# Performance work log

Hardware: AMD Instinct MI355X
Metric: run time of the kernel (lower is better)

The kernel has to match this reference:

```python
import jax, jax.numpy as jnp
import numpy as np

B, L, H, E, K = 64, 200, 256, 8, 2
LN_EPS = 1e-5

def setup_inputs() -> dict:
    key = jax.random.key(0)
    ks = jax.random.split(key, 24)
    r = lambda k, *s: jax.random.normal(k, s, dtype=jnp.float32)
    w = lambda k, *s: 0.02 * jax.random.normal(k, s, dtype=jnp.float32)
    return {
        'text_emb': r(ks[0], B, L, H),
        'img_emb': r(ks[1], B, L, H),
        'item_emb': r(ks[2], B, L, H),
        'noise_t': r(ks[3], B, L, H),
        'noise_i': r(ks[4], B, L, H),
        'W_mu_t': w(ks[5], H, H), 'b_mu_t': jnp.zeros((H,), jnp.float32),
        'W_sg_t': w(ks[6], H, H), 'b_sg_t': jnp.zeros((H,), jnp.float32),
        'W_mu_i': w(ks[7], H, H), 'b_mu_i': jnp.zeros((H,), jnp.float32),
        'W_sg_i': w(ks[8], H, H), 'b_sg_i': jnp.zeros((H,), jnp.float32),
        'W_gate': w(ks[9], H, E), 'b_gate': jnp.zeros((E,), jnp.float32),
        'W_texp': w(ks[10], E, H, H), 'b_texp': jnp.zeros((E, H), jnp.float32),
        'W_iexp': w(ks[11], E, H, H), 'b_iexp': jnp.zeros((E, H), jnp.float32),
        'W_fuse': w(ks[12], 2 * H, H), 'b_fuse': jnp.zeros((H,), jnp.float32),
        'ln_g': jnp.ones((H,), jnp.float32), 'ln_b': jnp.zeros((H,), jnp.float32),
    }

def _topk_routing(z, W_gate, b_gate):
    # softmax over experts, keep top-k, renormalize (matches torch scatter_ version)
    weights = jax.nn.softmax(z @ W_gate + b_gate, axis=-1)   # [B,L,E]
    top_w, idx = jax.lax.top_k(weights, K)                   # [B,L,K]
    sparse = jnp.sum(jax.nn.one_hot(idx, E, dtype=weights.dtype) * top_w[..., None], axis=-2)
    return sparse / (jnp.sum(sparse, axis=-1, keepdims=True) + 1e-8)

def _layernorm(x, g, b):
    mu = jnp.mean(x, axis=-1, keepdims=True)
    var = jnp.mean(jnp.square(x - mu), axis=-1, keepdims=True)
    return (x - mu) * jax.lax.rsqrt(var + LN_EPS) * g + b

def reference(text_emb, img_emb, item_emb, noise_t, noise_i,
              W_mu_t, b_mu_t, W_sg_t, b_sg_t, W_mu_i, b_mu_i, W_sg_i, b_sg_i,
              W_gate, b_gate, W_texp, b_texp, W_iexp, b_iexp,
              W_fuse, b_fuse, ln_g, ln_b):
    # VAE-style reparameterization per modality
    t_mu = text_emb @ W_mu_t + b_mu_t
    t_sigma = jnp.exp(text_emb @ W_sg_t + b_sg_t)
    i_mu = img_emb @ W_mu_i + b_mu_i
    i_sigma = jnp.exp(img_emb @ W_sg_i + b_sg_i)
    t_z = t_mu + t_sigma * noise_t
    i_z = i_mu + i_sigma * noise_i
    # top-k gating
    t_gate = _topk_routing(t_z, W_gate, b_gate)   # [B,L,E]
    i_gate = _topk_routing(i_z, W_gate, b_gate)
    # dense all-expert stack + gated combine
    t_experts = jnp.einsum('blh,ehd->bled', t_z, W_texp) + b_texp  # [B,L,E,H]
    t_out = jnp.einsum('bled,ble->bld', t_experts, t_gate)
    i_experts = jnp.einsum('blh,ehd->bled', i_z, W_iexp) + b_iexp
    i_out = jnp.einsum('bled,ble->bld', i_experts, i_gate)
    # fusion: Linear(2H->H) -> LayerNorm -> ReLU, residual with item_emb
    cat = jnp.concatenate([t_out, i_out], axis=-1)
    fused = jax.nn.relu(_layernorm(cat @ W_fuse + b_fuse, ln_g, ln_b))
    fusion = item_emb + fused
    return fusion, t_mu, t_sigma, i_mu, i_sigma
```

## Files before the change

kernel.cpp:

```cpp
#include <hip/hip_runtime.h>
#include <hip/hip_bf16.h>
#include <math.h>

#define NTOK 12800
#define HD 256
#define SOUT (NTOK * HD)

typedef __attribute__((ext_vector_type(8))) short short8_t;
typedef __attribute__((ext_vector_type(4))) float f32x4;

__device__ __forceinline__ unsigned short f2b(float f) {
    union { float f; unsigned u; } v; v.f = f;
    unsigned r = (v.u + 0x7FFFu + ((v.u >> 16) & 1u)) >> 16;
    return (unsigned short)r;
}
__device__ __forceinline__ float b2f(unsigned short s) {
    union { unsigned u; float f; } v; v.u = ((unsigned)s) << 16;
    return v.f;
}
__device__ __forceinline__ void glds16(const void* g, void* l) {
    __builtin_amdgcn_global_load_lds(
        (const __attribute__((address_space(1))) void*)g,
        (__attribute__((address_space(3))) void*)l, 16, 0, 0);
}
__device__ __forceinline__ short8_t add_bf16x8(short8_t a, short8_t b) {
    union { unsigned short u[8]; short8_t v; } ua, ub, r;
    ua.v = a; ub.v = b;
#pragma unroll
    for (int i = 0; i < 8; ++i) r.u[i] = f2b(b2f(ua.u[i]) + b2f(ub.u[i]));
    return r.v;
}
__device__ __forceinline__ void split8(const float* s, short8_t* hi, short8_t* lo) {
    const float4 v0 = *reinterpret_cast<const float4*>(s);
    const float4 v1 = *reinterpret_cast<const float4*>(s + 4);
    const float x[8] = { v0.x, v0.y, v0.z, v0.w, v1.x, v1.y, v1.z, v1.w };
    union { unsigned short u[8]; short8_t v; } qh, ql;
#pragma unroll
    for (int c = 0; c < 8; ++c) {
        qh.u[c] = f2b(x[c]);
        ql.u[c] = f2b(x[c] - b2f(qh.u[c]));
    }
    *hi = qh.v;
    *lo = ql.v;
}

__global__ __launch_bounds__(256) void prepW_kernel(
    const float* __restrict__ W_texp, const float* __restrict__ W_iexp,
    const float* __restrict__ W_mu_t, const float* __restrict__ W_sg_t,
    const float* __restrict__ W_mu_i, const float* __restrict__ W_sg_i,
    const float* __restrict__ W_fuse,
    unsigned short* __restrict__ wt_t, unsigned short* __restrict__ wt_i,
    unsigned short* __restrict__ wt_f,
    unsigned short* __restrict__ wpk_th, unsigned short* __restrict__ wpk_tl,
    unsigned short* __restrict__ wpk_ih, unsigned short* __restrict__ wpk_il)
{
    const int z = blockIdx.y;
    const float* src;
    unsigned short* dsth;
    unsigned short* dstl = nullptr;
    int dstride = 256, koff = 0, rowoff = 0;
    if (z < 8)       { src = W_texp + (size_t)z * 65536;       dsth = wt_t + (size_t)z * 65536; }
    else if (z < 16) { src = W_iexp + (size_t)(z - 8) * 65536; dsth = wt_i + (size_t)(z - 8) * 65536; }
    else if (z == 16){ src = W_mu_t; dsth = wpk_th; dstl = wpk_tl; }
    else if (z == 17){ src = W_sg_t; dsth = wpk_th; dstl = wpk_tl; rowoff = 256; }
    else if (z == 18){ src = W_mu_i; dsth = wpk_ih; dstl = wpk_il; }
    else if (z == 19){ src = W_sg_i; dsth = wpk_ih; dstl = wpk_il; rowoff = 256; }
    else if (z == 20){ src = W_fuse;         dsth = wt_f; dstride = 512; koff = 0;   }
    else             { src = W_fuse + 65536; dsth = wt_f; dstride = 512; koff = 256; }

    const int tk = (blockIdx.x >> 2) * 64;
    const int td = (blockIdx.x & 3) * 64;
    __shared__ float T[64][68];
    const int t = threadIdx.x;
    {
        const int r = t >> 2, c0 = (t & 3) * 16;
        const float* s = &src[(size_t)(tk + r) * 256 + td + c0];
#pragma unroll
        for (int j = 0; j < 4; ++j)
            *reinterpret_cast<float4*>(&T[r][c0 + j * 4]) =
                *reinterpret_cast<const float4*>(&s[j * 4]);
    }
    __syncthreads();
    {
        const int d = t & 63, kc = (t >> 6) * 16;
        union { unsigned short s[16]; short8_t v[2]; } uh, ul;
#pragma unroll
        for (int j = 0; j < 16; ++j) {
            const float x = T[kc + j][d];
            uh.s[j] = f2b(x);
            ul.s[j] = f2b(x - b2f(uh.s[j]));
        }
        unsigned short* p = &dsth[(size_t)(rowoff + td + d) * dstride + koff + tk + kc];
        *reinterpret_cast<short8_t*>(p) = uh.v[0];
        *reinterpret_cast<short8_t*>(p + 8) = uh.v[1];
        if (dstl) {
            unsigned short* q = &dstl[(size_t)(rowoff + td + d) * 256 + tk + kc];
            *reinterpret_cast<short8_t*>(q) = ul.v[0];
            *reinterpret_cast<short8_t*>(q + 8) = ul.v[1];
        }
    }
}

__global__ __launch_bounds__(256) void reparam_mfma_kernel(
    const float* __restrict__ text, const float* __restrict__ img,
    const unsigned short* __restrict__ wpk_th, const unsigned short* __restrict__ wpk_tl,
    const unsigned short* __restrict__ wpk_ih, const unsigned short* __restrict__ wpk_il,
    const float* __restrict__ b_mu_t, const float* __restrict__ b_sg_t,
    const float* __restrict__ b_mu_i, const float* __restrict__ b_sg_i,
    float* __restrict__ o_tmu, float* __restrict__ o_tsig,
    float* __restrict__ o_imu, float* __restrict__ o_isig)
{
    const int mod = blockIdx.z;
    const float* A = mod ? img : text;
    const unsigned short* Wh = mod ? wpk_ih : wpk_th;
    const unsigned short* Wl = mod ? wpk_il : wpk_tl;
    const float* bmu = mod ? b_mu_i : b_mu_t;
    const float* bsg = mod ? b_sg_i : b_sg_t;
    float* omu = mod ? o_imu : o_tmu;
    float* osg = mod ? o_isig : o_tsig;

    __shared__ __align__(16) unsigned short AhS[2][4][64][8];
    __shared__ __align__(16) unsigned short AlS[2][4][64][8];
    __shared__ __align__(16) unsigned short BhS[2][4][128][8];
    __shared__ __align__(16) unsigned short BlS[2][4][128][8];

    const int tid = threadIdx.x;
    const int lane = tid & 63;
    const int w = tid >> 6;
    const int wr = w >> 1, wc = w & 1;
    const int lg = lane >> 4;
    const int lr = lane & 15;
    const int m0 = blockIdx.x * 64;
    const int n0 = blockIdx.y * 128;

    const int ar = tid >> 2, akc = tid & 3;
    const int bn = tid >> 1, bk0 = (tid & 1) * 2;

    {
        short8_t h0, l0;
        split8(&A[(size_t)(m0 + ar) * HD + akc * 8], &h0, &l0);
        *reinterpret_cast<short8_t*>(&AhS[0][akc][ar][0]) = h0;
        *reinterpret_cast<short8_t*>(&AlS[0][akc][ar][0]) = l0;
#pragma unroll
        for (int j = 0; j < 2; ++j) {
            const int kc = bk0 + j;
            *reinterpret_cast<short8_t*>(&BhS[0][kc][bn][0]) =
                *reinterpret_cast<const short8_t*>(&Wh[(size_t)(n0 + bn) * HD + kc * 8]);
            *reinterpret_cast<short8_t*>(&BlS[0][kc][bn][0]) =
                *reinterpret_cast<const short8_t*>(&Wl[(size_t)(n0 + bn) * HD + kc * 8]);
        }
    }
    __syncthreads();

    f32x4 acc[2][4];
#pragma unroll
    for (int mi = 0; mi < 2; ++mi)
#pragma unroll
        for (int ni = 0; ni < 4; ++ni)
            acc[mi][ni] = (f32x4){0.f, 0.f, 0.f, 0.f};

    for (int ks = 0; ks < 8; ++ks) {
        const int cur = ks & 1;
        short8_t rah, ral, rbh[2], rbl[2];
        if (ks < 7) {
            const int k1 = (ks + 1) * 32;
            split8(&A[(size_t)(m0 + ar) * HD + k1 + akc * 8], &rah, &ral);
#pragma unroll
            for (int j = 0; j < 2; ++j) {
                const int kc = bk0 + j;
                rbh[j] = *reinterpret_cast<const short8_t*>(&Wh[(size_t)(n0 + bn) * HD + k1 + kc * 8]);
                rbl[j] = *reinterpret_cast<const short8_t*>(&Wl[(size_t)(n0 + bn) * HD + k1 + kc * 8]);
            }
        }
        short8_t ahf[2], alf[2], bhf[4], blf[4];
#pragma unroll
        for (int mi = 0; mi < 2; ++mi) {
            ahf[mi] = *reinterpret_cast<const short8_t*>(&AhS[cur][lg][wr * 32 + mi * 16 + lr][0]);
            alf[mi] = *reinterpret_cast<const short8_t*>(&AlS[cur][lg][wr * 32 + mi * 16 + lr][0]);
        }
#pragma unroll
        for (int ni = 0; ni < 4; ++ni) {
            bhf[ni] = *reinterpret_cast<const short8_t*>(&BhS[cur][lg][wc * 64 + ni * 16 + lr][0]);
            blf[ni] = *reinterpret_cast<const short8_t*>(&BlS[cur][lg][wc * 64 + ni * 16 + lr][0]);
        }
#pragma unroll
        for (int mi = 0; mi < 2; ++mi)
#pragma unroll
            for (int ni = 0; ni < 4; ++ni) {
                acc[mi][ni] = __builtin_amdgcn_mfma_f32_16x16x32_bf16(ahf[mi], bhf[ni], acc[mi][ni], 0, 0, 0);
                acc[mi][ni] = __builtin_amdgcn_mfma_f32_16x16x32_bf16(ahf[mi], blf[ni], acc[mi][ni], 0, 0, 0);
                acc[mi][ni] = __builtin_amdgcn_mfma_f32_16x16x32_bf16(alf[mi], bhf[ni], acc[mi][ni], 0, 0, 0);
            }
        if (ks < 7) {
            const int nxt = cur ^ 1;
            *reinterpret_cast<short8_t*>(&AhS[nxt][akc][ar][0]) = rah;
            *reinterpret_cast<short8_t*>(&AlS[nxt][akc][ar][0]) = ral;
#pragma unroll
            for (int j = 0; j < 2; ++j) {
                const int kc = bk0 + j;
                *reinterpret_cast<short8_t*>(&BhS[nxt][kc][bn][0]) = rbh[j];
                *reinterpret_cast<short8_t*>(&BlS[nxt][kc][bn][0]) = rbl[j];
            }
        }
        __syncthreads();
    }

    const bool is_sg = (n0 >= 256);
    float bv[4];
    int cc[4];
#pragma unroll
    for (int ni = 0; ni < 4; ++ni) {
        const int dpk = n0 + wc * 64 + ni * 16 + lr;
        cc[ni] = is_sg ? dpk - 256 : dpk;
        bv[ni] = is_sg ? bsg[cc[ni]] : bmu[cc[ni]];
    }
    float* outp = is_sg ? osg : omu;
#pragma unroll
    for (int mi = 0; mi < 2; ++mi)
#pragma unroll
        for (int r = 0; r < 4; ++r) {
            const int row = m0 + wr * 32 + mi * 16 + lg * 4 + r;
#pragma unroll
            for (int ni = 0; ni < 4; ++ni) {
                const float v = acc[mi][ni][r] + bv[ni];
                outp[(size_t)row * HD + cc[ni]] = is_sg ? expf(v) : v;
            }
        }
}

__global__ __launch_bounds__(256) void gate_kernel(
    const float* __restrict__ o_tmu, const float* __restrict__ o_tsig,
    const float* __restrict__ o_imu, const float* __restrict__ o_isig,
    const float* __restrict__ noise_t, const float* __restrict__ noise_i,
    const float* __restrict__ Wg, const float* __restrict__ bg,
    unsigned short* __restrict__ tzb, unsigned short* __restrict__ izb,
    unsigned* __restrict__ sel_e, float2* __restrict__ sel_w)
{
    const int mod = blockIdx.y;
    const float* mu    = mod ? o_imu  : o_tmu;
    const float* sig   = mod ? o_isig : o_tsig;
    const float* noise = mod ? noise_i : noise_t;
    unsigned short* zb = mod ? izb : tzb;

    const int lane = threadIdx.x & 63;
    const int n = blockIdx.x * 4 + (threadIdx.x >> 6);
    const size_t off = (size_t)n * HD + lane * 4;
    const float4 m4 = *reinterpret_cast<const float4*>(&mu[off]);
    const float4 s4 = *reinterpret_cast<const float4*>(&sig[off]);
    const float4 n4 = *reinterpret_cast<const float4*>(&noise[off]);
    const float zz[4] = { fmaf(s4.x, n4.x, m4.x), fmaf(s4.y, n4.y, m4.y),
                          fmaf(s4.z, n4.z, m4.z), fmaf(s4.w, n4.w, m4.w) };
    ushort4 zb4;
    zb4.x = f2b(zz[0]); zb4.y = f2b(zz[1]); zb4.z = f2b(zz[2]); zb4.w = f2b(zz[3]);
    *reinterpret_cast<ushort4*>(&zb[off]) = zb4;

    float lg[8];
#pragma unroll
    for (int e = 0; e < 8; ++e) lg[e] = 0.f;
#pragma unroll
    for (int i = 0; i < 4; ++i) {
        const float* wr = &Wg[(size_t)(lane * 4 + i) * 8];
        const float4 w0 = *reinterpret_cast<const float4*>(wr);
        const float4 w1 = *reinterpret_cast<const float4*>(wr + 4);
        lg[0] = fmaf(zz[i], w0.x, lg[0]); lg[1] = fmaf(zz[i], w0.y, lg[1]);
        lg[2] = fmaf(zz[i], w0.z, lg[2]); lg[3] = fmaf(zz[i], w0.w, lg[3]);
        lg[4] = fmaf(zz[i], w1.x, lg[4]); lg[5] = fmaf(zz[i], w1.y, lg[5]);
        lg[6] = fmaf(zz[i], w1.z, lg[6]); lg[7] = fmaf(zz[i], w1.w, lg[7]);
    }
#pragma unroll
    for (int off2 = 32; off2; off2 >>= 1)
#pragma unroll
        for (int e = 0; e < 8; ++e) lg[e] += __shfl_down(lg[e], off2);

    if (lane == 0) {
        float m = -1e30f;
#pragma unroll
        for (int e = 0; e < 8; ++e) { lg[e] += bg[e]; m = fmaxf(m, lg[e]); }
        float p[8], s = 0.f;
#pragma unroll
        for (int e = 0; e < 8; ++e) { p[e] = expf(lg[e] - m); s += p[e]; }
        const float inv_s = 1.f / s;
#pragma unroll
        for (int e = 0; e < 8; ++e) p[e] *= inv_s;
        int e1 = 0;
#pragma unroll
        for (int e = 1; e < 8; ++e) if (p[e] > p[e1]) e1 = e;
        int e2 = (e1 == 0) ? 1 : 0;
#pragma unroll
        for (int e = 0; e < 8; ++e) if (e != e1 && p[e] > p[e2]) e2 = e;
        const float denom = 1.f / (p[e1] + p[e2] + 1e-8f);
        sel_e[(size_t)mod * NTOK + n] = (unsigned)e1 | ((unsigned)e2 << 8);
        sel_w[(size_t)mod * NTOK + n] = make_float2(p[e1] * denom, p[e2] * denom);
    }
}

__global__ __launch_bounds__(1024) void compact_kernel(
    const unsigned* __restrict__ sel_e, const float2* __restrict__ sel_w,
    unsigned* __restrict__ idx_list, float* __restrict__ wgt_list,
    unsigned* __restrict__ cnt)
{
    const int seg = blockIdx.x;
    const int mod = seg >> 3;
    const unsigned e = (unsigned)(seg & 7);
    const int tid = threadIdx.x;
    const int wid = tid >> 6, lane = tid & 63;
    __shared__ unsigned wsum[16];

    unsigned off = 0;
    unsigned* dst_i = idx_list + (size_t)seg * NTOK;
    float* dst_w = wgt_list + (size_t)seg * NTOK;

    for (int chunk = 0; chunk < NTOK; chunk += 1024) {
        const int n = chunk + tid;
        const bool valid = (n < NTOK);
        unsigned se = 0;
        float2 wv = make_float2(0.f, 0.f);
        if (valid) {
            se = sel_e[(size_t)mod * NTOK + n];
            wv = sel_w[(size_t)mod * NTOK + n];
        }
#pragma unroll
        for (int slot = 0; slot < 2; ++slot) {
            const unsigned es = slot ? ((se >> 8) & 0xffu) : (se & 0xffu);
            const bool pred = valid && (es == e);
            const unsigned long long mask = __ballot(pred);
            if (lane == 0) wsum[wid] = (unsigned)__popcll(mask);
            __syncthreads();
            unsigned prefix = 0, total = 0;
#pragma unroll
            for (int wI = 0; wI < 16; ++wI) {
                const unsigned c = wsum[wI];
                if (wI < wid) prefix += c;
                total += c;
            }
            if (pred) {
                const unsigned long long lt = ((unsigned long long)1 << lane) - 1ull;
                const unsigned pos = off + prefix + (unsigned)__popcll(mask & lt);
                dst_i[pos] = (unsigned)(n * 2 + slot);
                dst_w[pos] = slot ? wv.y : wv.x;
            }
            off += total;
            __syncthreads();
        }
    }
    if (tid == 0) cnt[seg * 32] = off;
}

__global__ __launch_bounds__(256) void expert_sparse_kernel(
    const unsigned short* __restrict__ tzb, const unsigned short* __restrict__ izb,
    const unsigned short* __restrict__ wt_t, const unsigned short* __restrict__ wt_i,
    const float* __restrict__ bx_t, const float* __restrict__ bx_i,
    const unsigned* __restrict__ idx_list, const float* __restrict__ wgt_list,
    const unsigned* __restrict__ cnt,
    unsigned short* __restrict__ slot_t, unsigned short* __restrict__ slot_i)
{
    const int chunk = blockIdx.x;
    const int e  = blockIdx.y >> 1;
    const int nh = blockIdx.y & 1;
    const int mod = blockIdx.z;
    const int seg = mod * 8 + e;
    const unsigned cnt_e = cnt[seg * 32];
    if ((unsigned)(chunk * 128) >= cnt_e) return;

    const unsigned short* Zb = mod ? izb : tzb;
    const unsigned short* Wt = mod ? wt_i : wt_t;
    const float* bx = mod ? bx_i : bx_t;
    unsigned short* outp = mod ? slot_i : slot_t;
    const int n0 = nh * 128;
    const size_t sb = (size_t)seg * NTOK + (size_t)chunk * 128;

    __shared__ __align__(16) unsigned short Ab[2][512][8];
    __shared__ __align__(16) unsigned short Bb[2][512][8];
    __shared__ float gw[128];
    __shared__ unsigned il[128];

    const int tid = threadIdx.x;
    const int lane = tid & 63;
    const int w = tid >> 6;
    const int wr = w >> 1, wc = w & 1;
    const int lg = lane >> 4;
    const int lr = lane & 15;

    if (tid < 128) {
        const bool v = (unsigned)(chunk * 128 + tid) < cnt_e;
        il[tid] = v ? idx_list[sb + tid] : (unsigned)(2 * NTOK);
        gw[tid] = v ? wgt_list[sb + tid] : 0.f;
    }

    const int c0 = w * 64 + lane;
    const int row0 = c0 >> 2,         kc0 = c0 & 3;
    const int row1 = (c0 + 256) >> 2, kc1 = (c0 + 256) & 3;
    const unsigned i0 = ((unsigned)(chunk * 128 + row0) < cnt_e)
                        ? idx_list[sb + row0] : (unsigned)(2 * NTOK);
    const unsigned i1 = ((unsigned)(chunk * 128 + row1) < cnt_e)
                        ? idx_list[sb + row1] : (unsigned)(2 * NTOK);
    const size_t atok0 = (size_t)(i0 >> 1) * HD;
    const size_t atok1 = (size_t)(i1 >> 1) * HD;
    const unsigned short* We_ = Wt + (size_t)e * 65536 + (size_t)n0 * HD;

#define SSTAGE(buf, ks_)                                                       \
    {                                                                          \
        glds16(&Zb[atok0 + (ks_) * 32 + kc0 * 8], &Ab[buf][w * 64][0]);        \
        glds16(&Zb[atok1 + (ks_) * 32 + kc1 * 8], &Ab[buf][256 + w * 64][0]);  \
        glds16(&We_[(size_t)row0 * HD + (ks_) * 32 + kc0 * 8],                 \
               &Bb[buf][w * 64][0]);                                           \
        glds16(&We_[(size_t)row1 * HD + (ks_) * 32 + kc1 * 8],                 \
               &Bb[buf][256 + w * 64][0]);                                     \
    }

    SSTAGE(0, 0);
    __syncthreads();

    f32x4 acc[4][4];
#pragma unroll
    for (int mi = 0; mi < 4; ++mi)
#pragma unroll
        for (int ni = 0; ni < 4; ++ni)
            acc[mi][ni] = (f32x4){0.f, 0.f, 0.f, 0.f};

    for (int ks = 0; ks < 8; ++ks) {
        const int cur = ks & 1;
        if (ks < 7) SSTAGE(cur ^ 1, ks + 1);
        short8_t af[4], bf[4];
#pragma unroll
        for (int mi = 0; mi < 4; ++mi)
            af[mi] = *reinterpret_cast<const short8_t*>(
                &Ab[cur][(wr * 64 + mi * 16 + lr) * 4 + lg][0]);
#pragma unroll
        for (int ni = 0; ni < 4; ++ni)
            bf[ni] = *reinterpret_cast<const short8_t*>(
                &Bb[cur][(wc * 64 + ni * 16 + lr) * 4 + lg][0]);
#pragma unroll
        for (int mi = 0; mi < 4; ++mi)
#pragma unroll
            for (int ni = 0; ni < 4; ++ni)
                acc[mi][ni] = __builtin_amdgcn_mfma_f32_16x16x32_bf16(
                    af[mi], bf[ni], acc[mi][ni], 0, 0, 0);
        __syncthreads();
    }
#undef SSTAGE

    float bv[4];
#pragma unroll
    for (int ni = 0; ni < 4; ++ni)
        bv[ni] = bx[(size_t)e * HD + n0 + wc * 64 + ni * 16 + lr];
#pragma unroll
    for (int mi = 0; mi < 4; ++mi)
#pragma unroll
        for (int r = 0; r < 4; ++r) {
            const int row_local = wr * 64 + mi * 16 + lg * 4 + r;
            const float wv = gw[row_local];
            const size_t tb = (size_t)il[row_local] * HD;
#pragma unroll
            for (int ni = 0; ni < 4; ++ni)
                outp[tb + n0 + wc * 64 + ni * 16 + lr] =
                    f2b(wv * (acc[mi][ni][r] + bv[ni]));
        }
}

__global__ __launch_bounds__(256) void fusegemm_mfma_kernel(
    const unsigned short* __restrict__ slot_t, const unsigned short* __restrict__ slot_i,
    const unsigned short* __restrict__ wtf, const float* __restrict__ bfuse,
    float* __restrict__ fused)
{
    __shared__ __align__(16) unsigned short AS[2][8][64][8];
    __shared__ __align__(16) unsigned short BS[2][8][128][8];

    const int tid = threadIdx.x;
    const int lane = tid & 63;
    const int w = tid >> 6;
    const int wr = w >> 1, wc = w & 1;
    const int lg = lane >> 4;
    const int lr = lane & 15;
    const int m0 = blockIdx.x * 64;
    const int n0 = blockIdx.y * 128;

    const int ar = tid >> 2, akc0 = (tid & 3) * 2;
    const int bn = tid >> 1, bkc0 = (tid & 1) * 4;
    const size_t tb = (size_t)(m0 + ar) * 2 * HD;

    {
#pragma unroll
        for (int j = 0; j < 2; ++j) {
            const int kc = akc0 + j;
            const short8_t s0 = *reinterpret_cast<const short8_t*>(&slot_t[tb + kc * 8]);
            const short8_t s1 = *reinterpret_cast<const short8_t*>(&slot_t[tb + HD + kc * 8]);
            *reinterpret_cast<short8_t*>(&AS[0][kc][ar][0]) = add_bf16x8(s0, s1);
        }
#pragma unroll
        for (int j = 0; j < 4; ++j) {
            const int kc = bkc0 + j;
            *reinterpret_cast<short8_t*>(&BS[0][kc][bn][0]) =
                *reinterpret_cast<const short8_t*>(&wtf[(size_t)(n0 + bn) * 512 + kc * 8]);
        }
    }
    __syncthreads();

    f32x4 acc[2][4];
#pragma unroll
    for (int mi = 0; mi < 2; ++mi)
#pragma unroll
        for (int ni = 0; ni < 4; ++ni)
            acc[mi][ni] = (f32x4){0.f, 0.f, 0.f, 0.f};

    for (int ks = 0; ks < 8; ++ks) {
        const int cur = ks & 1;
        short8_t ra[2], rbv[4];
        if (ks < 7) {
            const int ks2 = ks + 1;
            const unsigned short* sp = (ks2 < 4) ? slot_t : slot_i;
            const int kloc = (ks2 & 3) * 64;
#pragma unroll
            for (int j = 0; j < 2; ++j) {
                const int kc = akc0 + j;
                const short8_t s0 = *reinterpret_cast<const short8_t*>(
                    &sp[tb + kloc + kc * 8]);
                const short8_t s1 = *reinterpret_cast<const short8_t*>(
                    &sp[tb + HD + kloc + kc * 8]);
                ra[j] = add_bf16x8(s0, s1);
            }
#pragma unroll
            for (int j = 0; j < 4; ++j) {
                const int kc = bkc0 + j;
                rbv[j] = *reinterpret_cast<const short8_t*>(
                    &wtf[(size_t)(n0 + bn) * 512 + ks2 * 64 + kc * 8]);
            }
        }
#pragma unroll
        for (int s = 0; s < 2; ++s) {
            short8_t af[2], bf[4];
#pragma unroll
            for (int mi = 0; mi < 2; ++mi)
                af[mi] = *reinterpret_cast<const short8_t*>(
                    &AS[cur][s * 4 + lg][wr * 32 + mi * 16 + lr][0]);
#pragma unroll
            for (int ni = 0; ni < 4; ++ni)
                bf[ni] = *reinterpret_cast<const short8_t*>(
                    &BS[cur][s * 4 + lg][wc * 64 + ni * 16 + lr][0]);
#pragma unroll
            for (int mi = 0; mi < 2; ++mi)
#pragma unroll
                for (int ni = 0; ni < 4; ++ni)
                    acc[mi][ni] = __builtin_amdgcn_mfma_f32_16x16x32_bf16(
                        af[mi], bf[ni], acc[mi][ni], 0, 0, 0);
        }
        if (ks < 7) {
            const int nxt = cur ^ 1;
#pragma unroll
            for (int j = 0; j < 2; ++j)
                *reinterpret_cast<short8_t*>(&AS[nxt][akc0 + j][ar][0]) = ra[j];
#pragma unroll
            for (int j = 0; j < 4; ++j)
                *reinterpret_cast<short8_t*>(&BS[nxt][bkc0 + j][bn][0]) = rbv[j];
        }
        __syncthreads();
    }

    float bv[4];
    int cc[4];
#pragma unroll
    for (int ni = 0; ni < 4; ++ni) {
        cc[ni] = n0 + wc * 64 + ni * 16 + lr;
        bv[ni] = bfuse[cc[ni]];
    }
#pragma unroll
    for (int mi = 0; mi < 2; ++mi)
#pragma unroll
        for (int r = 0; r < 4; ++r) {
            const int row = m0 + wr * 32 + mi * 16 + lg * 4 + r;
#pragma unroll
            for (int ni = 0; ni < 4; ++ni)
                fused[(size_t)row * HD + cc[ni]] = acc[mi][ni][r] + bv[ni];
        }
}

__global__ __launch_bounds__(256) void ln_relu_res_kernel(
    const float* __restrict__ fused, const float* __restrict__ g,
    const float* __restrict__ b, const float* __restrict__ item,
    float* __restrict__ fusion)
{
    const int lane = threadIdx.x & 63;
    const int n = blockIdx.x * 4 + (threadIdx.x >> 6);
    const size_t off = (size_t)n * HD + lane * 4;
    const float4 x = *reinterpret_cast<const float4*>(&fused[off]);
    float s = x.x + x.y + x.z + x.w;
    float ss = x.x * x.x + x.y * x.y + x.z * x.z + x.w * x.w;
#pragma unroll
    for (int o = 32; o; o >>= 1) { s += __shfl_xor(s, o); ss += __shfl_xor(ss, o); }
    const float mean = s * (1.f / 256.f);
    const float var = ss * (1.f / 256.f) - mean * mean;
    const float rstd = rsqrtf(var + 1e-5f);
    const float4 gg = *reinterpret_cast<const float4*>(&g[lane * 4]);
    const float4 bb = *reinterpret_cast<const float4*>(&b[lane * 4]);
    const float4 it = *reinterpret_cast<const float4*>(&item[off]);
    float4 o4;
    o4.x = fmaxf((x.x - mean) * rstd * gg.x + bb.x, 0.f) + it.x;
    o4.y = fmaxf((x.y - mean) * rstd * gg.y + bb.y, 0.f) + it.y;
    o4.z = fmaxf((x.z - mean) * rstd * gg.z + bb.z, 0.f) + it.z;
    o4.w = fmaxf((x.w - mean) * rstd * gg.w + bb.w, 0.f) + it.w;
    *reinterpret_cast<float4*>(&fusion[off]) = o4;
}

extern "C" void kernel_launch(void* const* d_in, const int* in_sizes, int n_in,
                              void* d_out, int out_size, void* d_ws, size_t ws_size,
                              hipStream_t stream)
{
    const float* text    = (const float*)d_in[0];
    const float* img     = (const float*)d_in[1];
    const float* item    = (const float*)d_in[2];
    const float* noise_t = (const float*)d_in[3];
    const float* noise_i = (const float*)d_in[4];
    const float* W_mu_t  = (const float*)d_in[5];
    const float* b_mu_t  = (const float*)d_in[6];
    const float* W_sg_t  = (const float*)d_in[7];
    const float* b_sg_t  = (const float*)d_in[8];
    const float* W_mu_i  = (const float*)d_in[9];
    const float* b_mu_i  = (const float*)d_in[10];
    const float* W_sg_i  = (const float*)d_in[11];
    const float* b_sg_i  = (const float*)d_in[12];
    const float* W_gate  = (const float*)d_in[13];
    const float* b_gate  = (const float*)d_in[14];
    const float* W_texp  = (const float*)d_in[15];
    const float* b_texp  = (const float*)d_in[16];
    const float* W_iexp  = (const float*)d_in[17];
    const float* b_iexp  = (const float*)d_in[18];
    const float* W_fuse  = (const float*)d_in[19];
    const float* b_fuse  = (const float*)d_in[20];
    const float* ln_g    = (const float*)d_in[21];
    const float* ln_b    = (const float*)d_in[22];

    float* out    = (float*)d_out;
    float* fusion = out;
    float* o_tmu  = out + (size_t)SOUT;
    float* o_tsig = out + (size_t)2 * SOUT;
    float* o_imu  = out + (size_t)3 * SOUT;
    float* o_isig = out + (size_t)4 * SOUT;

    const size_t SLOTPAD = (size_t)(2 * NTOK + 256) * HD;
    unsigned short* slot_t = (unsigned short*)d_ws;
    unsigned short* slot_i = slot_t + SLOTPAD;
    unsigned short* tzb    = slot_i + SLOTPAD;
    unsigned short* izb    = tzb + (size_t)SOUT;
    unsigned short* wt_t   = izb + (size_t)SOUT;
    unsigned short* wt_i   = wt_t + (size_t)8 * 65536;
    unsigned short* wt_f   = wt_i + (size_t)8 * 65536;
    unsigned short* wpk_th = wt_f + (size_t)131072;
    unsigned short* wpk_tl = wpk_th + (size_t)131072;
    unsigned short* wpk_ih = wpk_tl + (size_t)131072;
    unsigned short* wpk_il = wpk_ih + (size_t)131072;
    unsigned* idx_list = (unsigned*)(wpk_il + (size_t)131072);
    float*    wgt_list = (float*)(idx_list + (size_t)16 * NTOK);
    unsigned* cnt      = (unsigned*)(wgt_list + (size_t)16 * NTOK);
    unsigned* sel_e    = cnt + 512;
    float2*   sel_w    = (float2*)(sel_e + (size_t)2 * NTOK);

    float* fused = (float*)tzb;

    prepW_kernel<<<dim3(16, 22), 256, 0, stream>>>(
        W_texp, W_iexp, W_mu_t, W_sg_t, W_mu_i, W_sg_i, W_fuse,
        wt_t, wt_i, wt_f, wpk_th, wpk_tl, wpk_ih, wpk_il);

    reparam_mfma_kernel<<<dim3(NTOK / 64, 4, 2), 256, 0, stream>>>(
        text, img, wpk_th, wpk_tl, wpk_ih, wpk_il,
        b_mu_t, b_sg_t, b_mu_i, b_sg_i,
        o_tmu, o_tsig, o_imu, o_isig);

    gate_kernel<<<dim3(NTOK / 4, 2), 256, 0, stream>>>(
        o_tmu, o_tsig, o_imu, o_isig, noise_t, noise_i,
        W_gate, b_gate, tzb, izb, sel_e, sel_w);

    compact_kernel<<<16, 1024, 0, stream>>>(
        sel_e, sel_w, idx_list, wgt_list, cnt);

    expert_sparse_kernel<<<dim3(100, 16, 2), 256, 0, stream>>>(
        tzb, izb, wt_t, wt_i, b_texp, b_iexp,
        idx_list, wgt_list, cnt, slot_t, slot_i);

    fusegemm_mfma_kernel<<<dim3(NTOK / 64, 2), 256, 0, stream>>>(
        slot_t, slot_i, wt_f, b_fuse, fused);

    ln_relu_res_kernel<<<NTOK / 4, 256, 0, stream>>>(fused, ln_g, ln_b, item, fusion);
}
```

Baseline: 137.8 us.

## Fuse reparameterization into reparam GEMM epilogue by pairing mu and sigma columns

Each reparam GEMM block now computes matching mu and sigma column tiles (64 of each) rather than a 128-wide slice that is either all mu or all sigma. Because both values are in registers together, the epilogue computes z = mu + sigma*noise directly and writes z in fp32 and bf16. The gate kernel then reads only z instead of re-reading mu, sigma and noise. The A-tile LDS layout also changes to a flat per-thread chunk indexing. The cost is extra fp32 z writes into reused slot buffers and a scattered 2-byte bf16 store pattern in the epilogue.

```diff
diff --git a/kernel.cpp b/kernel.cpp
--- a/kernel.cpp
+++ b/kernel.cpp
@@ -107,20 +107,28 @@
     const unsigned short* __restrict__ wpk_ih, const unsigned short* __restrict__ wpk_il,
     const float* __restrict__ b_mu_t, const float* __restrict__ b_sg_t,
     const float* __restrict__ b_mu_i, const float* __restrict__ b_sg_i,
+    const float* __restrict__ noise_t, const float* __restrict__ noise_i,
     float* __restrict__ o_tmu, float* __restrict__ o_tsig,
-    float* __restrict__ o_imu, float* __restrict__ o_isig)
+    float* __restrict__ o_imu, float* __restrict__ o_isig,
+    float* __restrict__ z_t, float* __restrict__ z_i,
+    unsigned short* __restrict__ tzb, unsigned short* __restrict__ izb)
 {
     const int mod = blockIdx.z;
+    const int d0 = blockIdx.y * 64;
+    const int m0 = blockIdx.x * 64;
     const float* A = mod ? img : text;
     const unsigned short* Wh = mod ? wpk_ih : wpk_th;
     const unsigned short* Wl = mod ? wpk_il : wpk_tl;
-    const float* bmu = mod ? b_mu_i : b_mu_t;
-    const float* bsg = mod ? b_sg_i : b_sg_t;
+    const float* bmu   = mod ? b_mu_i : b_mu_t;
+    const float* bsg   = mod ? b_sg_i : b_sg_t;
+    const float* noise = mod ? noise_i : noise_t;
     float* omu = mod ? o_imu : o_tmu;
     float* osg = mod ? o_isig : o_tsig;
-
-    __shared__ __align__(16) unsigned short AhS[2][4][64][8];
-    __shared__ __align__(16) unsigned short AlS[2][4][64][8];
+    float* zf  = mod ? z_i : z_t;
+    unsigned short* zb = mod ? izb : tzb;
+
+    __shared__ __align__(16) unsigned short AhS[2][256][8];
+    __shared__ __align__(16) unsigned short AlS[2][256][8];
     __shared__ __align__(16) unsigned short BhS[2][4][128][8];
     __shared__ __align__(16) unsigned short BlS[2][4][128][8];
 
@@ -130,34 +138,35 @@
     const int wr = w >> 1, wc = w & 1;
     const int lg = lane >> 4;
     const int lr = lane & 15;
-    const int m0 = blockIdx.x * 64;
-    const int n0 = blockIdx.y * 128;
 
     const int ar = tid >> 2, akc = tid & 3;
     const int bn = tid >> 1, bk0 = (tid & 1) * 2;
+    const int brow = (bn < 64) ? (d0 + bn) : (256 + d0 + bn - 64);
 
     {
         short8_t h0, l0;
         split8(&A[(size_t)(m0 + ar) * HD + akc * 8], &h0, &l0);
-        *reinterpret_cast<short8_t*>(&AhS[0][akc][ar][0]) = h0;
-        *reinterpret_cast<short8_t*>(&AlS[0][akc][ar][0]) = l0;
+        *reinterpret_cast<short8_t*>(&AhS[0][tid][0]) = h0;
+        *reinterpret_cast<short8_t*>(&AlS[0][tid][0]) = l0;
 #pragma unroll
         for (int j = 0; j < 2; ++j) {
             const int kc = bk0 + j;
             *reinterpret_cast<short8_t*>(&BhS[0][kc][bn][0]) =
-                *reinterpret_cast<const short8_t*>(&Wh[(size_t)(n0 + bn) * HD + kc * 8]);
+                *reinterpret_cast<const short8_t*>(&Wh[(size_t)brow * HD + kc * 8]);
             *reinterpret_cast<short8_t*>(&BlS[0][kc][bn][0]) =
-                *reinterpret_cast<const short8_t*>(&Wl[(size_t)(n0 + bn) * HD + kc * 8]);
+                *reinterpret_cast<const short8_t*>(&Wl[(size_t)brow * HD + kc * 8]);
         }
     }
     __syncthreads();
 
-    f32x4 acc[2][4];
+    f32x4 accM[2][2], accS[2][2];
 #pragma unroll
     for (int mi = 0; mi < 2; ++mi)
 #pragma unroll
-        for (int ni = 0; ni < 4; ++ni)
-            acc[mi][ni] = (f32x4){0.f, 0.f, 0.f, 0.f};
+        for (int ni = 0; ni < 2; ++ni) {
+            accM[mi][ni] = (f32x4){0.f, 0.f, 0.f, 0.f};
+            accS[mi][ni] = (f32x4){0.f, 0.f, 0.f, 0.f};
+        }
 
     for (int ks = 0; ks < 8; ++ks) {
         const int cur = ks & 1;
@@ -168,33 +177,40 @@
 #pragma unroll
             for (int j = 0; j < 2; ++j) {
                 const int kc = bk0 + j;
-                rbh[j] = *reinterpret_cast<const short8_t*>(&Wh[(size_t)(n0 + bn) * HD + k1 + kc * 8]);
-                rbl[j] = *reinterpret_cast<const short8_t*>(&Wl[(size_t)(n0 + bn) * HD + k1 + kc * 8]);
-            }
-        }
-        short8_t ahf[2], alf[2], bhf[4], blf[4];
+                rbh[j] = *reinterpret_cast<const short8_t*>(&Wh[(size_t)brow * HD + k1 + kc * 8]);
+                rbl[j] = *reinterpret_cast<const short8_t*>(&Wl[(size_t)brow * HD + k1 + kc * 8]);
+            }
+        }
+        short8_t ahf[2], alf[2], bMh[2], bMl[2], bSh[2], bSl[2];
 #pragma unroll
         for (int mi = 0; mi < 2; ++mi) {
-            ahf[mi] = *reinterpret_cast<const short8_t*>(&AhS[cur][lg][wr * 32 + mi * 16 + lr][0]);
-            alf[mi] = *reinterpret_cast<const short8_t*>(&AlS[cur][lg][wr * 32 + mi * 16 + lr][0]);
-        }
-#pragma unroll
-        for (int ni = 0; ni < 4; ++ni) {
-            bhf[ni] = *reinterpret_cast<const short8_t*>(&BhS[cur][lg][wc * 64 + ni * 16 + lr][0]);
-            blf[ni] = *reinterpret_cast<const short8_t*>(&BlS[cur][lg][wc * 64 + ni * 16 + lr][0]);
+            const int ch = (wr * 32 + mi * 16 + lr) * 4 + lg;
+            ahf[mi] = *reinterpret_cast<const short8_t*>(&AhS[cur][ch][0]);
+            alf[mi] = *reinterpret_cast<const short8_t*>(&AlS[cur][ch][0]);
+        }
+#pragma unroll
+        for (int ni = 0; ni < 2; ++ni) {
+            const int cm = wc * 32 + ni * 16 + lr;
+            bMh[ni] = *reinterpret_cast<const short8_t*>(&BhS[cur][lg][cm][0]);
+            bMl[ni] = *reinterpret_cast<const short8_t*>(&BlS[cur][lg][cm][0]);
+            bSh[ni] = *reinterpret_cast<const short8_t*>(&BhS[cur][lg][64 + cm][0]);
+            bSl[ni] = *reinterpret_cast<const short8_t*>(&BlS[cur][lg][64 + cm][0]);
         }
 #pragma unroll
         for (int mi = 0; mi < 2; ++mi)
 #pragma unroll
-            for (int ni = 0; ni < 4; ++ni) {
-                acc[mi][ni] = __builtin_amdgcn_mfma_f32_16x16x32_bf16(ahf[mi], bhf[ni], acc[mi][ni], 0, 0, 0);
-                acc[mi][ni] = __builtin_amdgcn_mfma_f32_16x16x32_bf16(ahf[mi], blf[ni], acc[mi][ni], 0, 0, 0);
-                acc[mi][ni] = __builtin_amdgcn_mfma_f32_16x16x32_bf16(alf[mi], bhf[ni], acc[mi][ni], 0, 0, 0);
+            for (int ni = 0; ni < 2; ++ni) {
+                accM[mi][ni] = __builtin_amdgcn_mfma_f32_16x16x32_bf16(ahf[mi], bMh[ni], accM[mi][ni], 0, 0, 0);
+                accM[mi][ni] = __builtin_amdgcn_mfma_f32_16x16x32_bf16(ahf[mi], bMl[ni], accM[mi][ni], 0, 0, 0);
+                accM[mi][ni] = __builtin_amdgcn_mfma_f32_16x16x32_bf16(alf[mi], bMh[ni], accM[mi][ni], 0, 0, 0);
+                accS[mi][ni] = __builtin_amdgcn_mfma_f32_16x16x32_bf16(ahf[mi], bSh[ni], accS[mi][ni], 0, 0, 0);
+                accS[mi][ni] = __builtin_amdgcn_mfma_f32_16x16x32_bf16(ahf[mi], bSl[ni], accS[mi][ni], 0, 0, 0);
+                accS[mi][ni] = __builtin_amdgcn_mfma_f32_16x16x32_bf16(alf[mi], bSh[ni], accS[mi][ni], 0, 0, 0);
             }
         if (ks < 7) {
             const int nxt = cur ^ 1;
-            *reinterpret_cast<short8_t*>(&AhS[nxt][akc][ar][0]) = rah;
-            *reinterpret_cast<short8_t*>(&AlS[nxt][akc][ar][0]) = ral;
+            *reinterpret_cast<short8_t*>(&AhS[nxt][tid][0]) = rah;
+            *reinterpret_cast<short8_t*>(&AlS[nxt][tid][0]) = ral;
 #pragma unroll
             for (int j = 0; j < 2; ++j) {
                 const int kc = bk0 + j;
@@ -205,54 +221,46 @@
         __syncthreads();
     }
 
-    const bool is_sg = (n0 >= 256);
-    float bv[4];
-    int cc[4];
-#pragma unroll
-    for (int ni = 0; ni < 4; ++ni) {
-        const int dpk = n0 + wc * 64 + ni * 16 + lr;
-        cc[ni] = is_sg ? dpk - 256 : dpk;
-        bv[ni] = is_sg ? bsg[cc[ni]] : bmu[cc[ni]];
-    }
-    float* outp = is_sg ? osg : omu;
+    float bmv[2], bsv[2];
+    int cc[2];
+#pragma unroll
+    for (int ni = 0; ni < 2; ++ni) {
+        cc[ni] = d0 + wc * 32 + ni * 16 + lr;
+        bmv[ni] = bmu[cc[ni]];
+        bsv[ni] = bsg[cc[ni]];
+    }
 #pragma unroll
     for (int mi = 0; mi < 2; ++mi)
 #pragma unroll
         for (int r = 0; r < 4; ++r) {
             const int row = m0 + wr * 32 + mi * 16 + lg * 4 + r;
 #pragma unroll
-            for (int ni = 0; ni < 4; ++ni) {
-                const float v = acc[mi][ni][r] + bv[ni];
-                outp[(size_t)row * HD + cc[ni]] = is_sg ? expf(v) : v;
+            for (int ni = 0; ni < 2; ++ni) {
+                const size_t off = (size_t)row * HD + cc[ni];
+                const float mu = accM[mi][ni][r] + bmv[ni];
+                const float sg = expf(accS[mi][ni][r] + bsv[ni]);
+                const float z = fmaf(sg, noise[off], mu);
+                omu[off] = mu;
+                osg[off] = sg;
+                zf[off] = z;
+                zb[off] = f2b(z);
             }
         }
 }
 
 __global__ __launch_bounds__(256) void gate_kernel(
-    const float* __restrict__ o_tmu, const float* __restrict__ o_tsig,
-    const float* __restrict__ o_imu, const float* __restrict__ o_isig,
-    const float* __restrict__ noise_t, const float* __restrict__ noise_i,
+    const float* __restrict__ z_t, const float* __restrict__ z_i,
     const float* __restrict__ Wg, const float* __restrict__ bg,
-    unsigned short* __restrict__ tzb, unsigned short* __restrict__ izb,
     unsigned* __restrict__ sel_e, float2* __restrict__ sel_w)
 {
     const int mod = blockIdx.y;
-    const float* mu    = mod ? o_imu  : o_tmu;
-    const float* sig   = mod ? o_isig : o_tsig;
-    const float* noise = mod ? noise_i : noise_t;
-    unsigned short* zb = mod ? izb : tzb;
+    const float* zf = mod ? z_i : z_t;
 
     const int lane = threadIdx.x & 63;
     const int n = blockIdx.x * 4 + (threadIdx.x >> 6);
     const size_t off = (size_t)n * HD + lane * 4;
-    const float4 m4 = *reinterpret_cast<const float4*>(&mu[off]);
-    const float4 s4 = *reinterpret_cast<const float4*>(&sig[off]);
-    const float4 n4 = *reinterpret_cast<const float4*>(&noise[off]);
-    const float zz[4] = { fmaf(s4.x, n4.x, m4.x), fmaf(s4.y, n4.y, m4.y),
-                          fmaf(s4.z, n4.z, m4.z), fmaf(s4.w, n4.w, m4.w) };
-    ushort4 zb4;
-    zb4.x = f2b(zz[0]); zb4.y = f2b(zz[1]); zb4.z = f2b(zz[2]); zb4.w = f2b(zz[3]);
-    *reinterpret_cast<ushort4*>(&zb[off]) = zb4;
+    const float4 z4 = *reinterpret_cast<const float4*>(&zf[off]);
+    const float zz[4] = { z4.x, z4.y, z4.z, z4.w };
 
     float lg[8];
 #pragma unroll
@@ -654,6 +662,8 @@
     unsigned* sel_e    = cnt + 512;
     float2*   sel_w    = (float2*)(sel_e + (size_t)2 * NTOK);
 
+    float* z_t = (float*)slot_t;
+    float* z_i = (float*)slot_i;
     float* fused = (float*)tzb;
 
     prepW_kernel<<<dim3(16, 22), 256, 0, stream>>>(
@@ -662,12 +672,11 @@
 
     reparam_mfma_kernel<<<dim3(NTOK / 64, 4, 2), 256, 0, stream>>>(
         text, img, wpk_th, wpk_tl, wpk_ih, wpk_il,
-        b_mu_t, b_sg_t, b_mu_i, b_sg_i,
-        o_tmu, o_tsig, o_imu, o_isig);
+        b_mu_t, b_sg_t, b_mu_i, b_sg_i, noise_t, noise_i,
+        o_tmu, o_tsig, o_imu, o_isig, z_t, z_i, tzb, izb);
 
     gate_kernel<<<dim3(NTOK / 4, 2), 256, 0, stream>>>(
-        o_tmu, o_tsig, o_imu, o_isig, noise_t, noise_i,
-        W_gate, b_gate, tzb, izb, sel_e, sel_w);
+        z_t, z_i, W_gate, b_gate, sel_e, sel_w);
 
     compact_kernel<<<16, 1024, 0, stream>>>(
         sel_e, sel_w, idx_list, wgt_list, cnt);
```

New measurement: 140.0 us. About the same (+1.6%).

## Fuse LayerNorm, ReLU and residual into the fusion GEMM epilogue

Applied to the files above, without the earlier changes.

The fusion GEMM now computes full 256-wide output rows per block (32 rows × 256 cols) so LayerNorm statistics can be reduced in-block through shuffles and a small shared-memory exchange between the two column-half waves. The epilogue applies LN, ReLU and the item residual directly, which removes the fp32 intermediate write and re-read and one kernel launch. In exchange each block loads the whole W_fuse tile per k-step, so weight traffic per row is larger. Epilogue stores are also strided, not float4-vectorized as before.

```diff
diff --git a/kernel.cpp b/kernel.cpp
--- a/kernel.cpp
+++ b/kernel.cpp
@@ -458,13 +458,15 @@
         }
 }
 
-__global__ __launch_bounds__(256) void fusegemm_mfma_kernel(
+__global__ __launch_bounds__(256) void fusegemm_ln_kernel(
     const unsigned short* __restrict__ slot_t, const unsigned short* __restrict__ slot_i,
     const unsigned short* __restrict__ wtf, const float* __restrict__ bfuse,
-    float* __restrict__ fused)
+    const float* __restrict__ lng, const float* __restrict__ lnb,
+    const float* __restrict__ item, float* __restrict__ fusion)
 {
-    __shared__ __align__(16) unsigned short AS[2][8][64][8];
-    __shared__ __align__(16) unsigned short BS[2][8][128][8];
+    __shared__ __align__(16) unsigned short AS[2][8][32][8];
+    __shared__ __align__(16) unsigned short BS[2][8][256][8];
+    __shared__ float2 part[2][32];
 
     const int tid = threadIdx.x;
     const int lane = tid & 63;
@@ -472,133 +474,111 @@
     const int wr = w >> 1, wc = w & 1;
     const int lg = lane >> 4;
     const int lr = lane & 15;
-    const int m0 = blockIdx.x * 64;
-    const int n0 = blockIdx.y * 128;
-
-    const int ar = tid >> 2, akc0 = (tid & 3) * 2;
-    const int bn = tid >> 1, bkc0 = (tid & 1) * 4;
+    const int m0 = blockIdx.x * 32;
+
+    const int ar = tid >> 3, akc = tid & 7;
+    const int bn = tid;
     const size_t tb = (size_t)(m0 + ar) * 2 * HD;
 
     {
-#pragma unroll
-        for (int j = 0; j < 2; ++j) {
-            const int kc = akc0 + j;
-            const short8_t s0 = *reinterpret_cast<const short8_t*>(&slot_t[tb + kc * 8]);
-            const short8_t s1 = *reinterpret_cast<const short8_t*>(&slot_t[tb + HD + kc * 8]);
-            *reinterpret_cast<short8_t*>(&AS[0][kc][ar][0]) = add_bf16x8(s0, s1);
-        }
-#pragma unroll
-        for (int j = 0; j < 4; ++j) {
-            const int kc = bkc0 + j;
-            *reinterpret_cast<short8_t*>(&BS[0][kc][bn][0]) =
-                *reinterpret_cast<const short8_t*>(&wtf[(size_t)(n0 + bn) * 512 + kc * 8]);
-        }
+        const short8_t s0 = *reinterpret_cast<const short8_t*>(&slot_t[tb + akc * 8]);
+        const short8_t s1 = *reinterpret_cast<const short8_t*>(&slot_t[tb + HD + akc * 8]);
+        *reinterpret_cast<short8_t*>(&AS[0][akc][ar][0]) = add_bf16x8(s0, s1);
+#pragma unroll
+        for (int j = 0; j < 8; ++j)
+            *reinterpret_cast<short8_t*>(&BS[0][j][bn][0]) =
+                *reinterpret_cast<const short8_t*>(&wtf[(size_t)bn * 512 + j * 8]);
     }
     __syncthreads();
 
-    f32x4 acc[2][4];
-#pragma unroll
-    for (int mi = 0; mi < 2; ++mi)
-#pragma unroll
-        for (int ni = 0; ni < 4; ++ni)
-            acc[mi][ni] = (f32x4){0.f, 0.f, 0.f, 0.f};
+    f32x4 acc[8];
+#pragma unroll
+    for (int ni = 0; ni < 8; ++ni) acc[ni] = (f32x4){0.f, 0.f, 0.f, 0.f};
 
     for (int ks = 0; ks < 8; ++ks) {
         const int cur = ks & 1;
-        short8_t ra[2], rbv[4];
+        short8_t ra, rbv[8];
         if (ks < 7) {
             const int ks2 = ks + 1;
             const unsigned short* sp = (ks2 < 4) ? slot_t : slot_i;
             const int kloc = (ks2 & 3) * 64;
-#pragma unroll
-            for (int j = 0; j < 2; ++j) {
-                const int kc = akc0 + j;
-                const short8_t s0 = *reinterpret_cast<const short8_t*>(
-                    &sp[tb + kloc + kc * 8]);
-                const short8_t s1 = *reinterpret_cast<const short8_t*>(
-                    &sp[tb + HD + kloc + kc * 8]);
-                ra[j] = add_bf16x8(s0, s1);
+            const short8_t s0 = *reinterpret_cast<const short8_t*>(&sp[tb + kloc + akc * 8]);
+            const short8_t s1 = *reinterpret_cast<const short8_t*>(&sp[tb + HD + kloc + akc * 8]);
+            ra = add_bf16x8(s0, s1);
+#pragma unroll
+            for (int j = 0; j < 8; ++j)
+                rbv[j] = *reinterpret_cast<const short8_t*>(
+                    &wtf[(size_t)bn * 512 + ks2 * 64 + j * 8]);
+        }
+#pragma unroll
+        for (int s = 0; s < 2; ++s) {
+            const short8_t af = *reinterpret_cast<const short8_t*>(
+                &AS[cur][s * 4 + lg][wr * 16 + lr][0]);
+#pragma unroll
+            for (int ni = 0; ni < 8; ++ni) {
+                const short8_t bf = *reinterpret_cast<const short8_t*>(
+                    &BS[cur][s * 4 + lg][wc * 128 + ni * 16 + lr][0]);
+                acc[ni] = __builtin_amdgcn_mfma_f32_16x16x32_bf16(af, bf, acc[ni], 0, 0, 0);
             }
-#pragma unroll
-            for (int j = 0; j < 4; ++j) {
-                const int kc = bkc0 + j;
-                rbv[j] = *reinterpret_cast<const short8_t*>(
-                    &wtf[(size_t)(n0 + bn) * 512 + ks2 * 64 + kc * 8]);
-            }
-        }
-#pragma unroll
-        for (int s = 0; s < 2; ++s) {
-            short8_t af[2], bf[4];
-#pragma unroll
-            for (int mi = 0; mi < 2; ++mi)
-                af[mi] = *reinterpret_cast<const short8_t*>(
-                    &AS[cur][s * 4 + lg][wr * 32 + mi * 16 + lr][0]);
-#pragma unroll
-            for (int ni = 0; ni < 4; ++ni)
-                bf[ni] = *reinterpret_cast<const short8_t*>(
-                    &BS[cur][s * 4 + lg][wc * 64 + ni * 16 + lr][0]);
-#pragma unroll
-            for (int mi = 0; mi < 2; ++mi)
-#pragma unroll
-                for (int ni = 0; ni < 4; ++ni)
-                    acc[mi][ni] = __builtin_amdgcn_mfma_f32_16x16x32_bf16(
-                        af[mi], bf[ni], acc[mi][ni], 0, 0, 0);
         }
         if (ks < 7) {
             const int nxt = cur ^ 1;
-#pragma unroll
-            for (int j = 0; j < 2; ++j)
-                *reinterpret_cast<short8_t*>(&AS[nxt][akc0 + j][ar][0]) = ra[j];
-#pragma unroll
-            for (int j = 0; j < 4; ++j)
-                *reinterpret_cast<short8_t*>(&BS[nxt][bkc0 + j][bn][0]) = rbv[j];
+            *reinterpret_cast<short8_t*>(&AS[nxt][akc][ar][0]) = ra;
+#pragma unroll
+            for (int j = 0; j < 8; ++j)
+                *reinterpret_cast<short8_t*>(&BS[nxt][j][bn][0]) = rbv[j];
         }
         __syncthreads();
     }
 
-    float bv[4];
-    int cc[4];
-#pragma unroll
-    for (int ni = 0; ni < 4; ++ni) {
-        cc[ni] = n0 + wc * 64 + ni * 16 + lr;
-        bv[ni] = bfuse[cc[ni]];
-    }
-#pragma unroll
-    for (int mi = 0; mi < 2; ++mi)
-#pragma unroll
-        for (int r = 0; r < 4; ++r) {
-            const int row = m0 + wr * 32 + mi * 16 + lg * 4 + r;
-#pragma unroll
-            for (int ni = 0; ni < 4; ++ni)
-                fused[(size_t)row * HD + cc[ni]] = acc[mi][ni][r] + bv[ni];
-        }
-}
-
-__global__ __launch_bounds__(256) void ln_relu_res_kernel(
-    const float* __restrict__ fused, const float* __restrict__ g,
-    const float* __restrict__ b, const float* __restrict__ item,
-    float* __restrict__ fusion)
-{
-    const int lane = threadIdx.x & 63;
-    const int n = blockIdx.x * 4 + (threadIdx.x >> 6);
-    const size_t off = (size_t)n * HD + lane * 4;
-    const float4 x = *reinterpret_cast<const float4*>(&fused[off]);
-    float s = x.x + x.y + x.z + x.w;
-    float ss = x.x * x.x + x.y * x.y + x.z * x.z + x.w * x.w;
-#pragma unroll
-    for (int o = 32; o; o >>= 1) { s += __shfl_xor(s, o); ss += __shfl_xor(ss, o); }
-    const float mean = s * (1.f / 256.f);
-    const float var = ss * (1.f / 256.f) - mean * mean;
-    const float rstd = rsqrtf(var + 1e-5f);
-    const float4 gg = *reinterpret_cast<const float4*>(&g[lane * 4]);
-    const float4 bb = *reinterpret_cast<const float4*>(&b[lane * 4]);
-    const float4 it = *reinterpret_cast<const float4*>(&item[off]);
-    float4 o4;
-    o4.x = fmaxf((x.x - mean) * rstd * gg.x + bb.x, 0.f) + it.x;
-    o4.y = fmaxf((x.y - mean) * rstd * gg.y + bb.y, 0.f) + it.y;
-    o4.z = fmaxf((x.z - mean) * rstd * gg.z + bb.z, 0.f) + it.z;
-    o4.w = fmaxf((x.w - mean) * rstd * gg.w + bb.w, 0.f) + it.w;
-    *reinterpret_cast<float4*>(&fusion[off]) = o4;
+    int cc[8];
+    float bvv[8];
+#pragma unroll
+    for (int ni = 0; ni < 8; ++ni) {
+        cc[ni] = wc * 128 + ni * 16 + lr;
+        bvv[ni] = bfuse[cc[ni]];
+    }
+#pragma unroll
+    for (int r = 0; r < 4; ++r) {
+        const int row_l = wr * 16 + lg * 4 + r;
+        float s = 0.f, ss = 0.f;
+#pragma unroll
+        for (int ni = 0; ni < 8; ++ni) {
+            const float v = acc[ni][r] + bvv[ni];
+            s += v;
+            ss = fmaf(v, v, ss);
+        }
+#pragma unroll
+        for (int o = 1; o < 16; o <<= 1) {
+            s += __shfl_xor(s, o);
+            ss += __shfl_xor(ss, o);
+        }
+        if (lr == 0) part[wc][row_l] = make_float2(s, ss);
+    }
+    __syncthreads();
+
+    float lgv[8], lbv[8];
+#pragma unroll
+    for (int ni = 0; ni < 8; ++ni) {
+        lgv[ni] = lng[cc[ni]];
+        lbv[ni] = lnb[cc[ni]];
+    }
+#pragma unroll
+    for (int r = 0; r < 4; ++r) {
+        const int row_l = wr * 16 + lg * 4 + r;
+        const int row = m0 + row_l;
+        const float2 p0 = part[0][row_l];
+        const float2 p1 = part[1][row_l];
+        const float mean = (p0.x + p1.x) * (1.f / 256.f);
+        const float var = (p0.y + p1.y) * (1.f / 256.f) - mean * mean;
+        const float rstd = rsqrtf(var + 1e-5f);
+#pragma unroll
+        for (int ni = 0; ni < 8; ++ni) {
+            const size_t off = (size_t)row * HD + cc[ni];
+            const float v = acc[ni][r] + bvv[ni];
+            fusion[off] = fmaxf((v - mean) * rstd * lgv[ni] + lbv[ni], 0.f) + item[off];
+        }
+    }
 }
 
 extern "C" void kernel_launch(void* const* d_in, const int* in_sizes, int n_in,
@@ -654,8 +634,6 @@
     unsigned* sel_e    = cnt + 512;
     float2*   sel_w    = (float2*)(sel_e + (size_t)2 * NTOK);
 
-    float* fused = (float*)tzb;
-
     prepW_kernel<<<dim3(16, 22), 256, 0, stream>>>(
         W_texp, W_iexp, W_mu_t, W_sg_t, W_mu_i, W_sg_i, W_fuse,
         wt_t, wt_i, wt_f, wpk_th, wpk_tl, wpk_ih, wpk_il);
@@ -676,8 +654,6 @@
         tzb, izb, wt_t, wt_i, b_texp, b_iexp,
         idx_list, wgt_list, cnt, slot_t, slot_i);
 
-    fusegemm_mfma_kernel<<<dim3(NTOK / 64, 2), 256, 0, stream>>>(
-        slot_t, slot_i, wt_f, b_fuse, fused);
-
-    ln_relu_res_kernel<<<NTOK / 4, 256, 0, stream>>>(fused, ln_g, ln_b, item, fusion);
-}
+    fusegemm_ln_kernel<<<NTOK / 32, 256, 0, stream>>>(
+        slot_t, slot_i, wt_f, b_fuse, ln_g, ln_b, item, fusion);
+}
```

New measurement: 140.5 us. About the same (+2.0%).
